# Kernel optimization log

Hardware: AMD Instinct MI355X
Metric: run time of the kernel (lower is better)

The kernel has to match this reference:

```python
import jax, jax.numpy as jnp
import numpy as np

N = 200000   # nodes
E = 6400000  # edges
F = 128      # input node features
H = 6        # hiddenSize (module constant)
C = 10       # num_classes
G = 64       # graphs in batch


def setup_inputs() -> dict:
    key = jax.random.key(0)
    ks = jax.random.split(key, 7)
    x = jax.random.normal(ks[0], (N, F), dtype=jnp.float32)
    edge_index = jax.random.randint(ks[1], (2, E), 0, N, dtype=jnp.int32)
    batch = jnp.sort(jax.random.randint(ks[2], (N,), 0, G, dtype=jnp.int32))
    W1 = jax.random.normal(ks[3], (F, H), dtype=jnp.float32) * (1.0 / np.sqrt(F))
    b1 = jnp.zeros((H,), dtype=jnp.float32)
    W2 = jax.random.normal(ks[4], (H, C), dtype=jnp.float32) * (1.0 / np.sqrt(H))
    b2 = jnp.zeros((C,), dtype=jnp.float32)
    return {"x": x, "edge_index": edge_index, "batch": batch,
            "W1": W1, "b1": b1, "W2": W2, "b2": b2}


def _gcn_conv(x, W, b, row, col, dis):
    # PyG GCNConv: h = x W; out = D^{-1/2}(A+I)D^{-1/2} h + b
    h = x @ W                                      # [N, out]
    norm = dis[row] * dis[col]                     # [E] edge normalization
    msg = norm[:, None] * h[row]                   # gather from source nodes
    agg = jax.ops.segment_sum(msg, col, num_segments=N)  # scatter-add to targets
    # self-loop term: norm = dis[i]*dis[i]
    return agg + (dis * dis)[:, None] * h + b


def reference(x, edge_index, batch, W1, b1, W2, b2):
    row, col = edge_index[0], edge_index[1]
    # degree after adding self-loops (edge_weight = 1)
    deg = jax.ops.segment_sum(jnp.ones((E,), dtype=x.dtype), col, num_segments=N) + 1.0
    dis = jax.lax.rsqrt(deg)                       # deg^{-1/2}

    h = _gcn_conv(x, W1, b1, row, col, dis)
    h = jax.nn.relu(h)
    # dropout is identity in inference mode
    h = _gcn_conv(h, W2, b2, row, col, dis)        # [N, C]

    # global mean pool over each graph
    sums = jax.ops.segment_sum(h, batch, num_segments=G)                  # [G, C]
    cnts = jax.ops.segment_sum(jnp.ones((N,), dtype=h.dtype), batch, num_segments=G)
    pooled = sums / jnp.maximum(cnts, 1.0)[:, None]
    return jax.nn.log_softmax(pooled, axis=1)      # [G, C]
```

## Files before the change

### kernel.cpp

```cpp
#include <hip/hip_runtime.h>
#include <math.h>

#define N_NODES 200000
#define N_EDGES 6400000
#define F_IN    128
#define H_HID   6
#define C_OUT   10
#define G_BATCH 64

#define TILE_E  8192
#define NT      ((N_EDGES + TILE_E - 1) / TILE_E)
#define EPT     16
#define BSH     9
#define BNODES  512
#define NBUCK   ((N_NODES + BNODES - 1) / BNODES)
#define BCAP    17408
#define XBLK    512
#define NXB     ((N_NODES + XBLK - 1) / XBLK)

__device__ __forceinline__ unsigned short f2bf(float f) {
    unsigned u = __float_as_uint(f);
    u += 0x7fff + ((u >> 16) & 1);
    return (unsigned short)(u >> 16);
}
__device__ __forceinline__ unsigned pack2(float a, float b) {
    return (unsigned)f2bf(a) | ((unsigned)f2bf(b) << 16);
}
__device__ __forceinline__ float bf_lo(unsigned u) { return __uint_as_float(u << 16); }
__device__ __forceinline__ float bf_hi(unsigned u) { return __uint_as_float(u & 0xffff0000u); }

__global__ __launch_bounds__(512, 8) void megaA_kernel(const int* __restrict__ row,
                                                       const int* __restrict__ col,
                                                       const float* __restrict__ x,
                                                       const float* __restrict__ W1,
                                                       int* __restrict__ gcur,
                                                       int* __restrict__ binned,
                                                       float* __restrict__ xacc, int E) {
    __shared__ int sortbuf[TILE_E];
    __shared__ int cnt[512];
    __shared__ int pos[513];
    __shared__ int lbase[512];
    __shared__ int wtot[8];
    int tid = threadIdx.x;

    if (blockIdx.x >= NT) {
        float* w = (float*)sortbuf;
        for (int i = tid; i < F_IN * H_HID; i += 512) w[i] = W1[i];
        __syncthreads();
        int n = (blockIdx.x - NT) * XBLK + tid;
        if (n >= N_NODES) return;
        float acc[H_HID] = {0.f, 0.f, 0.f, 0.f, 0.f, 0.f};
        const float4* xr = (const float4*)(x + (size_t)n * F_IN);
#pragma unroll 4
        for (int f4 = 0; f4 < F_IN / 4; ++f4) {
            float4 v = xr[f4];
            int f = f4 * 4;
#pragma unroll
            for (int j = 0; j < H_HID; ++j) {
                acc[j] += v.x * w[(f + 0) * H_HID + j] + v.y * w[(f + 1) * H_HID + j]
                        + v.z * w[(f + 2) * H_HID + j] + v.w * w[(f + 3) * H_HID + j];
            }
        }
#pragma unroll
        for (int j = 0; j < H_HID; ++j) xacc[j * N_NODES + n] = acc[j];
        return;
    }

    int t = blockIdx.x;
    int base = t * TILE_E;
    int tile_n = min(TILE_E, E - base);

    cnt[tid] = 0;
    __syncthreads();

    int myval[EPT];
    int myb[EPT];
    int ebase = base + tid * EPT;
    if (ebase + EPT <= E) {
        const int4* c4 = (const int4*)(col + ebase);
        const int4* r4 = (const int4*)(row + ebase);
#pragma unroll
        for (int q = 0; q < EPT / 4; ++q) {
            int4 c = c4[q];
            int4 r = r4[q];
            int k = q * 4;
            myval[k + 0] = ((c.x & (BNODES - 1)) << 18) | r.x;  myb[k + 0] = c.x >> BSH;
            myval[k + 1] = ((c.y & (BNODES - 1)) << 18) | r.y;  myb[k + 1] = c.y >> BSH;
            myval[k + 2] = ((c.z & (BNODES - 1)) << 18) | r.z;  myb[k + 2] = c.z >> BSH;
            myval[k + 3] = ((c.w & (BNODES - 1)) << 18) | r.w;  myb[k + 3] = c.w >> BSH;
        }
#pragma unroll
        for (int k = 0; k < EPT; ++k) atomicAdd(&cnt[myb[k]], 1);
    } else {
#pragma unroll
        for (int k = 0; k < EPT; ++k) {
            int e = ebase + k;
            if (e < E) {
                int c = col[e];
                myval[k] = ((c & (BNODES - 1)) << 18) | row[e];
                myb[k] = c >> BSH;
                atomicAdd(&cnt[myb[k]], 1);
            } else {
                myb[k] = -1;
            }
        }
    }
    __syncthreads();

    int c = cnt[tid];
    int v = c;
    int lane = tid & 63, wid = tid >> 6;
#pragma unroll
    for (int off = 1; off < 64; off <<= 1) {
        int u = __shfl_up(v, off);
        if (lane >= off) v += u;
    }
    if (lane == 63) wtot[wid] = v;
    __syncthreads();
    if (tid == 0) {
        int running = 0;
#pragma unroll
        for (int i = 0; i < 8; ++i) { int w2 = wtot[i]; wtot[i] = running; running += w2; }
    }
    __syncthreads();
    int incl = v + wtot[wid];
    int excl = incl - c;
    pos[tid] = excl;
    cnt[tid] = excl;
    if (tid == 511) pos[512] = incl;
    if (tid < NBUCK) {
        lbase[tid] = tid * BCAP + (c ? atomicAdd(&gcur[tid], c) : 0);
    }
    __syncthreads();

#pragma unroll
    for (int k = 0; k < EPT; ++k) {
        if (myb[k] >= 0) {
            int p = atomicAdd(&cnt[myb[k]], 1);
            sortbuf[p] = myval[k];
        }
    }
    __syncthreads();

    for (int i = tid; i < tile_n; i += 512) {
        int lo = 0, hi = NBUCK - 1;
        while (lo < hi) {
            int mid = (lo + hi + 1) >> 1;
            if (pos[mid] <= i) lo = mid; else hi = mid - 1;
        }
        binned[lbase[lo] + (i - pos[lo])] = sortbuf[i];
    }
}

__global__ __launch_bounds__(1024) void passB2_kernel(const int* __restrict__ gcur,
                                                      const int* __restrict__ binned,
                                                      const float* __restrict__ xacc,
                                                      int* __restrict__ deg,
                                                      uint4* __restrict__ h1b) {
    __shared__ int cnt[512];
    int b = blockIdx.x, tid = threadIdx.x;
    int bb = b * BCAP, be = bb + gcur[b];
    if (tid < 512) cnt[tid] = 0;
    __syncthreads();
    int e = bb + tid;
    for (; e + 3072 < be; e += 4096) {
        int p0 = binned[e], p1 = binned[e + 1024], p2 = binned[e + 2048], p3 = binned[e + 3072];
        atomicAdd(&cnt[p0 >> 18], 1); atomicAdd(&cnt[p1 >> 18], 1);
        atomicAdd(&cnt[p2 >> 18], 1); atomicAdd(&cnt[p3 >> 18], 1);
    }
    for (; e < be; e += 1024) atomicAdd(&cnt[binned[e] >> 18], 1);
    __syncthreads();
    if (tid < 512) {
        int n = (b << BSH) + tid;
        if (n < N_NODES) {
            int dv = cnt[tid];
            deg[n] = dv;
            float d = rsqrtf((float)dv + 1.0f);
            float a0 = xacc[0 * N_NODES + n], a1 = xacc[1 * N_NODES + n];
            float a2 = xacc[2 * N_NODES + n], a3 = xacc[3 * N_NODES + n];
            float a4 = xacc[4 * N_NODES + n], a5 = xacc[5 * N_NODES + n];
            uint4 o;
            o.x = pack2(d * a0, d * a1);
            o.y = pack2(d * a2, d * a3);
            o.z = pack2(d * a4, d * a5);
            o.w = __float_as_uint(d);
            h1b[n] = o;
        }
    }
}

#define DEG_SCAN(INCL)                                                          \
    {                                                                           \
        int n0 = (b << BSH) + tid;                                              \
        int v0 = (tid < 512 && n0 < N_NODES) ? deg[n0] : 0;                     \
        int v = v0;                                                             \
        int lane = tid & 63, wid = tid >> 6;                                    \
        _Pragma("unroll")                                                       \
        for (int off = 1; off < 64; off <<= 1) {                                \
            int u = __shfl_up(v, off);                                          \
            if (lane >= off) v += u;                                            \
        }                                                                       \
        if (wid < 8 && lane == 63) wtot[wid] = v;                               \
        __syncthreads();                                                        \
        if (tid == 0) {                                                         \
            int running = 0;                                                    \
            _Pragma("unroll")                                                   \
            for (int i = 0; i < 8; ++i) { int w2 = wtot[i]; wtot[i] = running; running += w2; } \
        }                                                                       \
        __syncthreads();                                                        \
        if (tid < 512) cnt[tid] = v + wtot[wid] - (INCL ? 0 : v0);              \
    }                                                                           \
    __syncthreads();

#define GATHER_BODY(TBL)                                                        \
    float a[H_HID] = {0.f, 0.f, 0.f, 0.f, 0.f, 0.f};                            \
    {                                                                           \
        int ee = s + sub;                                                       \
        for (; ee + 24 < e_end; ee += 32) {                                     \
            int i0 = stage[ee], i1 = stage[ee + 8];                             \
            int i2 = stage[ee + 16], i3 = stage[ee + 24];                       \
            uint4 v0 = TBL[i0], v1 = TBL[i1], v2 = TBL[i2], v3 = TBL[i3];       \
            a[0] += (bf_lo(v0.x) + bf_lo(v1.x)) + (bf_lo(v2.x) + bf_lo(v3.x));  \
            a[1] += (bf_hi(v0.x) + bf_hi(v1.x)) + (bf_hi(v2.x) + bf_hi(v3.x));  \
            a[2] += (bf_lo(v0.y) + bf_lo(v1.y)) + (bf_lo(v2.y) + bf_lo(v3.y));  \
            a[3] += (bf_hi(v0.y) + bf_hi(v1.y)) + (bf_hi(v2.y) + bf_hi(v3.y));  \
            a[4] += (bf_lo(v0.z) + bf_lo(v1.z)) + (bf_lo(v2.z) + bf_lo(v3.z));  \
            a[5] += (bf_hi(v0.z) + bf_hi(v1.z)) + (bf_hi(v2.z) + bf_hi(v3.z));  \
        }                                                                       \
        for (; ee < e_end; ee += 8) {                                           \
            uint4 vv = TBL[stage[ee]];                                          \
            a[0] += bf_lo(vv.x); a[1] += bf_hi(vv.x);                           \
            a[2] += bf_lo(vv.y); a[3] += bf_hi(vv.y);                           \
            a[4] += bf_lo(vv.z); a[5] += bf_hi(vv.z);                           \
        }                                                                       \
    }                                                                           \
    _Pragma("unroll")                                                           \
    for (int j = 0; j < H_HID; ++j) {                                           \
        _Pragma("unroll")                                                       \
        for (int off = 4; off > 0; off >>= 1) a[j] += __shfl_xor(a[j], off);    \
    }

__global__ __launch_bounds__(1024) void bg1_kernel(const int* __restrict__ gcur,
                                                   const int* __restrict__ binned,
                                                   const int* __restrict__ deg,
                                                   const uint4* __restrict__ h1b,
                                                   const float* __restrict__ b1,
                                                   int* __restrict__ csr,
                                                   uint4* __restrict__ rs) {
    __shared__ int stage[BCAP];
    __shared__ int cnt[512];
    __shared__ int wtot[8];
    int b = blockIdx.x, tid = threadIdx.x;
    int bb = b * BCAP, be = bb + gcur[b];
    int total = be - bb;

    DEG_SCAN(0)

    {
        int e = bb + tid;
        for (; e + 3072 < be; e += 4096) {
            int p0 = binned[e], p1 = binned[e + 1024];
            int p2 = binned[e + 2048], p3 = binned[e + 3072];
            int s0 = atomicAdd(&cnt[p0 >> 18], 1); stage[s0] = p0 & 0x3FFFF;
            int s1 = atomicAdd(&cnt[p1 >> 18], 1); stage[s1] = p1 & 0x3FFFF;
            int s2 = atomicAdd(&cnt[p2 >> 18], 1); stage[s2] = p2 & 0x3FFFF;
            int s3 = atomicAdd(&cnt[p3 >> 18], 1); stage[s3] = p3 & 0x3FFFF;
        }
        for (; e < be; e += 1024) {
            int p = binned[e];
            int s = atomicAdd(&cnt[p >> 18], 1); stage[s] = p & 0x3FFFF;
        }
    }
    __syncthreads();

    for (int i = tid * 4; i + 3 < total; i += 4096)
        *(int4*)(csr + bb + i) = *(const int4*)(stage + i);
    {
        int b4 = total & ~3, r = total - b4;
        if (tid < r) csr[bb + b4 + tid] = stage[b4 + tid];
    }

    int sub = tid & 7, grp = tid >> 3;
    for (int ch = 0; ch < 4; ++ch) {
        int ln = ch * 128 + grp;
        int n = (b << BSH) + ln;
        int s = ln ? cnt[ln - 1] : 0;
        int e_end = cnt[ln];
        GATHER_BODY(h1b)
        if (sub == 0 && n < N_NODES) {
            uint4 self = h1b[n];
            float d = __uint_as_float(self.w);
            float sf[H_HID] = {bf_lo(self.x), bf_hi(self.x), bf_lo(self.y),
                               bf_hi(self.y), bf_lo(self.z), bf_hi(self.z)};
            float r[H_HID];
#pragma unroll
            for (int j = 0; j < H_HID; ++j) {
                float vv = d * (a[j] + sf[j]) + b1[j];
                r[j] = d * (vv > 0.f ? vv : 0.f);
            }
            uint4 o;
            o.x = pack2(r[0], r[1]);
            o.y = pack2(r[2], r[3]);
            o.z = pack2(r[4], r[5]);
            o.w = self.w;
            rs[n] = o;
        }
    }
}

__global__ __launch_bounds__(1024) void bg2_kernel(const int* __restrict__ gcur,
                                                   const int* __restrict__ deg,
                                                   const int* __restrict__ csr,
                                                   const uint4* __restrict__ rs,
                                                   const float* __restrict__ W2,
                                                   const int* __restrict__ batch,
                                                   float* __restrict__ sums) {
    __shared__ int stage[BCAP];
    __shared__ int cnt[512];
    __shared__ int wtot[8];
    __shared__ float w2s[H_HID * C_OUT];
    __shared__ float nv[128][C_OUT + 1];
    __shared__ int lg[128];
    __shared__ float gacc[2][C_OUT];
    __shared__ int sg0;
    int b = blockIdx.x, tid = threadIdx.x;
    int bb = b * BCAP;
    int total = gcur[b];
    if (tid < H_HID * C_OUT) w2s[tid] = W2[tid];
    if (tid < 2 * C_OUT) ((float*)gacc)[tid] = 0.f;
    if (tid == 0) sg0 = batch[b << BSH];

    for (int i = tid * 4; i + 3 < total; i += 4096)
        *(int4*)(stage + i) = *(const int4*)(csr + bb + i);
    {
        int b4 = total & ~3, r = total - b4;
        if (tid < r) stage[b4 + tid] = csr[bb + b4 + tid];
    }

    DEG_SCAN(1)

    int sub = tid & 7, grp = tid >> 3;
    for (int ch = 0; ch < 4; ++ch) {
        int ln = ch * 128 + grp;
        int n = (b << BSH) + ln;
        int s = ln ? cnt[ln - 1] : 0;
        int e_end = cnt[ln];
        GATHER_BODY(rs)
        uint4 self = {0u, 0u, 0u, 0u};
        if (n < N_NODES) self = rs[n];
        float d = (n < N_NODES) ? __uint_as_float(self.w) : 0.f;
        float t[H_HID] = {a[0] + bf_lo(self.x), a[1] + bf_hi(self.x),
                          a[2] + bf_lo(self.y), a[3] + bf_hi(self.y),
                          a[4] + bf_lo(self.z), a[5] + bf_hi(self.z)};
        {
            float accv = 0.f;
#pragma unroll
            for (int j = 0; j < H_HID; ++j) accv += t[j] * w2s[j * C_OUT + sub];
            nv[grp][sub] = d * accv;
            if (sub < 2) {
                float accv2 = 0.f;
#pragma unroll
                for (int j = 0; j < H_HID; ++j) accv2 += t[j] * w2s[j * C_OUT + sub + 8];
                nv[grp][sub + 8] = d * accv2;
            }
        }
        if (sub == 0) lg[grp] = (n < N_NODES) ? batch[n] : sg0;
        __syncthreads();
        if (tid < 80) {
            int seg = tid / C_OUT, cc = tid - seg * C_OUT;
            int g = -1; float av = 0.f;
            for (int i = 0; i < 16; ++i) {
                int wdx = seg * 16 + i;
                int gw = lg[wdx];
                if (gw != g) {
                    if (g >= 0) {
                        int r2 = g - sg0;
                        if (r2 < 2) atomicAdd(&gacc[r2][cc], av);
                        else atomicAdd(&sums[g * C_OUT + cc], av);
                    }
                    g = gw; av = 0.f;
                }
                av += nv[wdx][cc];
            }
            int r2 = g - sg0;
            if (r2 < 2) atomicAdd(&gacc[r2][cc], av);
            else atomicAdd(&sums[g * C_OUT + cc], av);
        }
        __syncthreads();
    }
    if (tid < 2 * C_OUT) {
        int r2 = tid / C_OUT, cc = tid - r2 * C_OUT;
        int g = sg0 + r2;
        if (g < G_BATCH) atomicAdd(&sums[g * C_OUT + cc], gacc[r2][cc]);
    }
}

__global__ void pool_finish_kernel(const float* __restrict__ sums, const int* __restrict__ batch,
                                   const float* __restrict__ b2, float* __restrict__ out) {
    int g = threadIdx.x;
    if (g >= G_BATCH) return;
    int lo = 0, hi = N_NODES;
    while (lo < hi) { int mid = (lo + hi) >> 1; if (batch[mid] < g) lo = mid + 1; else hi = mid; }
    int c0 = lo;
    hi = N_NODES;
    while (lo < hi) { int mid = (lo + hi) >> 1; if (batch[mid] < g + 1) lo = mid + 1; else hi = mid; }
    float inv = 1.0f / fmaxf((float)(lo - c0), 1.0f);
    float v[C_OUT], m = -INFINITY;
#pragma unroll
    for (int c = 0; c < C_OUT; ++c) {
        v[c] = sums[g * C_OUT + c] * inv + b2[c];
        m = fmaxf(m, v[c]);
    }
    float s = 0.f;
#pragma unroll
    for (int c = 0; c < C_OUT; ++c) s += expf(v[c] - m);
    float lse = m + logf(s);
#pragma unroll
    for (int c = 0; c < C_OUT; ++c) out[g * C_OUT + c] = v[c] - lse;
}

extern "C" void kernel_launch(void* const* d_in, const int* in_sizes, int n_in,
                              void* d_out, int out_size, void* d_ws, size_t ws_size,
                              hipStream_t stream) {
    const float* x   = (const float*)d_in[0];
    const int* ei    = (const int*)d_in[1];
    const int* row   = ei;
    const int* col   = ei + N_EDGES;
    const int* batch = (const int*)d_in[2];
    const float* W1  = (const float*)d_in[3];
    const float* b1  = (const float*)d_in[4];
    const float* W2  = (const float*)d_in[5];
    const float* b2  = (const float*)d_in[6];
    float* out = (float*)d_out;

    char* p = (char*)d_ws;
    float* sums   = (float*)p;  p += (size_t)G_BATCH * C_OUT * 4;
    int*   gcur   = (int*)p;    p += (size_t)400 * 4;
    int*   deg    = (int*)p;    p += (size_t)N_NODES * 4;
    int*   binned = (int*)p;    p += (size_t)NBUCK * BCAP * 4;
    int*   csr    = (int*)p;    p += (size_t)NBUCK * BCAP * 4;
    float* xacc   = (float*)p;  p += (size_t)H_HID * N_NODES * 4;
    uint4* h1b    = (uint4*)p;  p += (size_t)N_NODES * 16;
    uint4* rs     = (uint4*)p;

    hipMemsetAsync(sums, 0, (size_t)G_BATCH * C_OUT * 4 + 400 * 4, stream);

    megaA_kernel  <<<NT + NXB, 512, 0, stream>>>(row, col, x, W1, gcur, binned, xacc, N_EDGES);
    passB2_kernel <<<NBUCK, 1024, 0, stream>>>(gcur, binned, xacc, deg, h1b);
    bg1_kernel    <<<NBUCK, 1024, 0, stream>>>(gcur, binned, deg, h1b, b1, csr, rs);
    bg2_kernel    <<<NBUCK, 1024, 0, stream>>>(gcur, deg, csr, rs, W2, batch, sums);
    pool_finish_kernel<<<1, 64, 0, stream>>>(sums, batch, b2, out);
}
```

Before: 318.0 us.

## Scatter binned edges directly to global and read CSR indices from global in bg2

In the binning kernel, the shared-memory staging sort, prefix scan and binary-search copy-out are removed. Each edge is now written straight to its global bucket slot, claimed through per-bucket atomic offsets. In bg2, the CSR index slice is no longer staged into shared memory; the gather reads indices directly from global memory. This cuts shared-memory use and several barriers, which could raise occupancy, but it makes the global writes in the binning pass scattered instead of coalesced and adds global loads to the gather.

```diff
diff --git a/kernel.cpp b/kernel.cpp
--- a/kernel.cpp
+++ b/kernel.cpp
@@ -36,16 +36,12 @@
                                                        int* __restrict__ gcur,
                                                        int* __restrict__ binned,
                                                        float* __restrict__ xacc, int E) {
-    __shared__ int sortbuf[TILE_E];
     __shared__ int cnt[512];
-    __shared__ int pos[513];
-    __shared__ int lbase[512];
-    __shared__ int wtot[8];
+    __shared__ float wbuf[F_IN * H_HID];
     int tid = threadIdx.x;
 
     if (blockIdx.x >= NT) {
-        float* w = (float*)sortbuf;
-        for (int i = tid; i < F_IN * H_HID; i += 512) w[i] = W1[i];
+        for (int i = tid; i < F_IN * H_HID; i += 512) wbuf[i] = W1[i];
         __syncthreads();
         int n = (blockIdx.x - NT) * XBLK + tid;
         if (n >= N_NODES) return;
@@ -57,8 +53,8 @@
             int f = f4 * 4;
 #pragma unroll
             for (int j = 0; j < H_HID; ++j) {
-                acc[j] += v.x * w[(f + 0) * H_HID + j] + v.y * w[(f + 1) * H_HID + j]
-                        + v.z * w[(f + 2) * H_HID + j] + v.w * w[(f + 3) * H_HID + j];
+                acc[j] += v.x * wbuf[(f + 0) * H_HID + j] + v.y * wbuf[(f + 1) * H_HID + j]
+                        + v.z * wbuf[(f + 2) * H_HID + j] + v.w * wbuf[(f + 3) * H_HID + j];
             }
         }
 #pragma unroll
@@ -68,7 +64,6 @@
 
     int t = blockIdx.x;
     int base = t * TILE_E;
-    int tile_n = min(TILE_E, E - base);
 
     cnt[tid] = 0;
     __syncthreads();
@@ -107,29 +102,10 @@
     }
     __syncthreads();
 
-    int c = cnt[tid];
-    int v = c;
-    int lane = tid & 63, wid = tid >> 6;
-#pragma unroll
-    for (int off = 1; off < 64; off <<= 1) {
-        int u = __shfl_up(v, off);
-        if (lane >= off) v += u;
-    }
-    if (lane == 63) wtot[wid] = v;
-    __syncthreads();
-    if (tid == 0) {
-        int running = 0;
-#pragma unroll
-        for (int i = 0; i < 8; ++i) { int w2 = wtot[i]; wtot[i] = running; running += w2; }
-    }
-    __syncthreads();
-    int incl = v + wtot[wid];
-    int excl = incl - c;
-    pos[tid] = excl;
-    cnt[tid] = excl;
-    if (tid == 511) pos[512] = incl;
-    if (tid < NBUCK) {
-        lbase[tid] = tid * BCAP + (c ? atomicAdd(&gcur[tid], c) : 0);
+    {
+        int c = cnt[tid];
+        int slot = tid * BCAP + (c ? atomicAdd(&gcur[tid], c) : 0);
+        cnt[tid] = slot;
     }
     __syncthreads();
 
@@ -137,18 +113,8 @@
     for (int k = 0; k < EPT; ++k) {
         if (myb[k] >= 0) {
             int p = atomicAdd(&cnt[myb[k]], 1);
-            sortbuf[p] = myval[k];
-        }
-    }
-    __syncthreads();
-
-    for (int i = tid; i < tile_n; i += 512) {
-        int lo = 0, hi = NBUCK - 1;
-        while (lo < hi) {
-            int mid = (lo + hi + 1) >> 1;
-            if (pos[mid] <= i) lo = mid; else hi = mid - 1;
-        }
-        binned[lbase[lo] + (i - pos[lo])] = sortbuf[i];
+            binned[p] = myval[k];
+        }
     }
 }
 
@@ -240,6 +206,34 @@
         for (int off = 4; off > 0; off >>= 1) a[j] += __shfl_xor(a[j], off);    \
     }
 
+#define GATHER_BODY_G(TBL, IDXP)                                                \
+    float a[H_HID] = {0.f, 0.f, 0.f, 0.f, 0.f, 0.f};                            \
+    {                                                                           \
+        int ee = s + sub;                                                       \
+        for (; ee + 24 < e_end; ee += 32) {                                     \
+            int i0 = IDXP[ee], i1 = IDXP[ee + 8];                               \
+            int i2 = IDXP[ee + 16], i3 = IDXP[ee + 24];                         \
+            uint4 v0 = TBL[i0], v1 = TBL[i1], v2 = TBL[i2], v3 = TBL[i3];       \
+            a[0] += (bf_lo(v0.x) + bf_lo(v1.x)) + (bf_lo(v2.x) + bf_lo(v3.x));  \
+            a[1] += (bf_hi(v0.x) + bf_hi(v1.x)) + (bf_hi(v2.x) + bf_hi(v3.x));  \
+            a[2] += (bf_lo(v0.y) + bf_lo(v1.y)) + (bf_lo(v2.y) + bf_lo(v3.y));  \
+            a[3] += (bf_hi(v0.y) + bf_hi(v1.y)) + (bf_hi(v2.y) + bf_hi(v3.y));  \
+            a[4] += (bf_lo(v0.z) + bf_lo(v1.z)) + (bf_lo(v2.z) + bf_lo(v3.z));  \
+            a[5] += (bf_hi(v0.z) + bf_hi(v1.z)) + (bf_hi(v2.z) + bf_hi(v3.z));  \
+        }                                                                       \
+        for (; ee < e_end; ee += 8) {                                           \
+            uint4 vv = TBL[IDXP[ee]];                                           \
+            a[0] += bf_lo(vv.x); a[1] += bf_hi(vv.x);                           \
+            a[2] += bf_lo(vv.y); a[3] += bf_hi(vv.y);                           \
+            a[4] += bf_lo(vv.z); a[5] += bf_hi(vv.z);                           \
+        }                                                                       \
+    }                                                                           \
+    _Pragma("unroll")                                                           \
+    for (int j = 0; j < H_HID; ++j) {                                           \
+        _Pragma("unroll")                                                       \
+        for (int off = 4; off > 0; off >>= 1) a[j] += __shfl_xor(a[j], off);    \
+    }
+
 __global__ __launch_bounds__(1024) void bg1_kernel(const int* __restrict__ gcur,
                                                    const int* __restrict__ binned,
                                                    const int* __restrict__ deg,
@@ -315,7 +309,6 @@
                                                    const float* __restrict__ W2,
                                                    const int* __restrict__ batch,
                                                    float* __restrict__ sums) {
-    __shared__ int stage[BCAP];
     __shared__ int cnt[512];
     __shared__ int wtot[8];
     __shared__ float w2s[H_HID * C_OUT];
@@ -325,17 +318,10 @@
     __shared__ int sg0;
     int b = blockIdx.x, tid = threadIdx.x;
     int bb = b * BCAP;
-    int total = gcur[b];
+    const int* idx = csr + bb;
     if (tid < H_HID * C_OUT) w2s[tid] = W2[tid];
     if (tid < 2 * C_OUT) ((float*)gacc)[tid] = 0.f;
     if (tid == 0) sg0 = batch[b << BSH];
-
-    for (int i = tid * 4; i + 3 < total; i += 4096)
-        *(int4*)(stage + i) = *(const int4*)(csr + bb + i);
-    {
-        int b4 = total & ~3, r = total - b4;
-        if (tid < r) stage[b4 + tid] = csr[bb + b4 + tid];
-    }
 
     DEG_SCAN(1)
 
@@ -345,7 +331,7 @@
         int n = (b << BSH) + ln;
         int s = ln ? cnt[ln - 1] : 0;
         int e_end = cnt[ln];
-        GATHER_BODY(rs)
+        GATHER_BODY_G(rs, idx)
         uint4 self = {0u, 0u, 0u, 0u};
         if (n < N_NODES) self = rs[n];
         float d = (n < N_NODES) ? __uint_as_float(self.w) : 0.f;
```

Result: slower. 335.5 us (+5.5%).
